# Kernel tuning notes

Measured on AMD Instinct MI355X. Metric: run time of the kernel, lower is better.

## Reference

```python
import jax, jax.numpy as jnp
import numpy as np
from jax import lax

BN_EPS = 1e-5

def _dw_conv_bn(img, w, g, b, mu, var):
    # img: [B,C,H,W], w: [C,1,3,3] depthwise (feature_group_count=C), stride 1, pad 1
    C = img.shape[1]
    y = lax.conv_general_dilated(img, w, (1, 1), 'SAME',
                                 dimension_numbers=('NCHW', 'OIHW', 'NCHW'),
                                 feature_group_count=C)
    scale = (g / jnp.sqrt(var + BN_EPS))[None, :, None, None]
    return y * scale + (b - mu * g / jnp.sqrt(var + BN_EPS))[None, :, None, None]


def setup_inputs() -> dict:
    key = jax.random.key(0)
    B, H, W, C, Co = 32, 28, 28, 192, 192
    T = 1 + H * W
    ks = jax.random.split(key, 8)
    x = jax.random.normal(ks[0], (B, T, C), dtype=jnp.float32)
    conv_w = jax.random.normal(ks[1], (3, C, 1, 3, 3), dtype=jnp.float32) * 0.1
    bn_scale = 1.0 + 0.1 * jax.random.normal(ks[2], (3, C), dtype=jnp.float32)
    bn_bias = 0.1 * jax.random.normal(ks[3], (3, C), dtype=jnp.float32)
    bn_mean = 0.1 * jax.random.normal(ks[4], (3, C), dtype=jnp.float32)
    bn_var = jax.random.uniform(ks[5], (3, C), dtype=jnp.float32, minval=0.5, maxval=1.5)
    w_qkv = jax.random.normal(ks[6], (3, Co, C), dtype=jnp.float32) / np.sqrt(C)
    kp, kb = jax.random.split(ks[7])
    w_proj = jax.random.normal(kp, (Co, Co), dtype=jnp.float32) / np.sqrt(Co)
    b_proj = 0.01 * jax.random.normal(kb, (Co,), dtype=jnp.float32)
    return {"x": x, "conv_w": conv_w, "bn_scale": bn_scale, "bn_bias": bn_bias,
            "bn_mean": bn_mean, "bn_var": bn_var, "w_qkv": w_qkv,
            "w_proj": w_proj, "b_proj": b_proj, "h": H, "w": W, "num_heads": 3}


def reference(x, conv_w, bn_scale, bn_bias, bn_mean, bn_var, w_qkv, w_proj, b_proj, h, w, num_heads):
    B, T, C = x.shape
    Co = w_proj.shape[0]
    scale = Co ** (-0.5)  # NOTE: module scales by dim_out^-0.5, not per-head
    cls_tok, tok = x[:, :1], x[:, 1:]
    img = tok.reshape(B, h, w, C).transpose(0, 3, 1, 2)  # b (h w) c -> b c h w
    qkv = []
    for i in range(3):  # q, k, v conv projections (depthwise conv + BN inference)
        y = _dw_conv_bn(img, conv_w[i], bn_scale[i], bn_bias[i], bn_mean[i], bn_var[i])
        y = y.reshape(B, C, h * w).transpose(0, 2, 1)  # b c h w -> b (h w) c
        y = jnp.concatenate([cls_tok, y], axis=1)      # prepend cls token
        qkv.append(jnp.einsum('btc,oc->bto', y, w_qkv[i]))
    d = Co // num_heads
    q, k, v = (t.reshape(B, T, num_heads, d).transpose(0, 2, 1, 3) for t in qkv)
    attn = jnp.einsum('bhld,bhtd->bhlt', q, k) * scale
    attn = jax.nn.softmax(attn, axis=-1)
    out = jnp.einsum('bhlt,bhtd->bhld', attn, v)
    out = out.transpose(0, 2, 1, 3).reshape(B, T, Co)
    return out @ w_proj.T + b_proj
```

## Files before the change

kernel.cpp:

```cpp
#include <hip/hip_runtime.h>

#define B_   32
#define Hh   28
#define Ww   28
#define Cc   192
#define T_   785
#define BT_  (B_ * T_)
#define BTC_ ((size_t)BT_ * Cc)
#define SCALE2 0.10412163388f

typedef __attribute__((ext_vector_type(8))) __bf16 bf16x8;
typedef __attribute__((ext_vector_type(4))) __bf16 bf16x4;
typedef __attribute__((ext_vector_type(4))) float  f32x4;

__device__ __forceinline__ int imin(int a, int b) { return a < b ? a : b; }

__global__ void wcvt_k(const float* __restrict__ wq, const float* __restrict__ wp,
                       __bf16* __restrict__ dst) {
  int i = blockIdx.x * 256 + threadIdx.x;
  float v = (i < 3 * Cc * Cc) ? wq[i] : wp[i - 3 * Cc * Cc];
  dst[i] = (__bf16)v;
}

__global__ __launch_bounds__(192) void conv3_bn_k(
    const float* __restrict__ x, const float* __restrict__ cw,
    const float* __restrict__ g, const float* __restrict__ bb,
    const float* __restrict__ mu, const float* __restrict__ var,
    __bf16* __restrict__ y)
{
  const int c = threadIdx.x;
  const int h0 = blockIdx.x * 2;
  const int b = blockIdx.y;
  float w9[3][9], sc[3], sh[3];
#pragma unroll
  for (int br = 0; br < 3; ++br) {
    sc[br] = g[br * Cc + c] * rsqrtf(var[br * Cc + c] + 1e-5f);
    sh[br] = bb[br * Cc + c] - mu[br * Cc + c] * sc[br];
#pragma unroll
    for (int k = 0; k < 9; ++k) w9[br][k] = cw[(br * Cc + c) * 9 + k];
  }
  const float* xb = x + (size_t)b * T_ * Cc;
  if (h0 == 0) {
#pragma unroll
    for (int br = 0; br < 3; ++br)
      y[br * BTC_ + (size_t)b * T_ * Cc + c] = (__bf16)xb[c];
  }
  float c0[4], c1[4], c2[4];
#pragma unroll
  for (int r = 0; r < 4; ++r) {
    int rr = h0 - 1 + r;
    c0[r] = 0.f;
    c1[r] = (rr >= 0 && rr < Hh) ? xb[(size_t)(1 + rr * Ww) * Cc + c] : 0.f;
  }
  for (int col = 0; col < Ww; ++col) {
#pragma unroll
    for (int r = 0; r < 4; ++r) {
      int rr = h0 - 1 + r, ci = col + 1;
      c2[r] = (rr >= 0 && rr < Hh && ci < Ww)
                ? xb[(size_t)(1 + rr * Ww + ci) * Cc + c] : 0.f;
    }
#pragma unroll
    for (int ro = 0; ro < 2; ++ro) {
      size_t orow = (size_t)(b * T_ + 1 + (h0 + ro) * Ww + col) * Cc + c;
#pragma unroll
      for (int br = 0; br < 3; ++br) {
        float acc = c0[ro+0]*w9[br][0] + c1[ro+0]*w9[br][1] + c2[ro+0]*w9[br][2]
                  + c0[ro+1]*w9[br][3] + c1[ro+1]*w9[br][4] + c2[ro+1]*w9[br][5]
                  + c0[ro+2]*w9[br][6] + c1[ro+2]*w9[br][7] + c2[ro+2]*w9[br][8];
        y[br * BTC_ + orow] = (__bf16)(acc * sc[br] + sh[br]);
      }
    }
#pragma unroll
    for (int r = 0; r < 4; ++r) { c0[r] = c1[r]; c1[r] = c2[r]; }
  }
}

template <int MODE>
__global__ __launch_bounds__(256) void gemm_bf16(
    const __bf16* __restrict__ A0, const __bf16* __restrict__ W0,
    const float* __restrict__ bias, void* __restrict__ outp)
{
  __shared__ __bf16 As[128][72];
  __shared__ __bf16 Bs[64][72];
  const int z = blockIdx.z;
  const __bf16* A  = A0 + (MODE == 0 ? (size_t)z * BTC_ : 0);
  const __bf16* Bw = W0 + (MODE == 0 ? (size_t)z * Cc * Cc : 0);
  const float oscale = (MODE == 0 && z == 0) ? SCALE2 : 1.0f;
  const int tid = threadIdx.x;
  const int wid = tid >> 6, l = tid & 63, c = l & 15, g = l >> 4;
  const int wm = wid >> 1, wn = wid & 1;
  const int m0 = blockIdx.x * 128, n0 = blockIdx.y * 64;
  const int ar = tid >> 1, ah = tid & 1;
  const int br2 = tid >> 2, bq = tid & 3;

  f32x4 acc[4][2];
#pragma unroll
  for (int i = 0; i < 4; ++i)
#pragma unroll
    for (int j = 0; j < 2; ++j) acc[i][j] = (f32x4)(0.f);

  const __bf16* ap = A + (size_t)imin(m0 + ar, BT_ - 1) * Cc + ah * 32;
  const __bf16* bp = Bw + (size_t)(n0 + br2) * Cc + bq * 16;
  uint4 a0 = *(const uint4*)(ap + 0);
  uint4 a1 = *(const uint4*)(ap + 8);
  uint4 a2 = *(const uint4*)(ap + 16);
  uint4 a3 = *(const uint4*)(ap + 24);
  uint4 b0 = *(const uint4*)(bp + 0);
  uint4 b1 = *(const uint4*)(bp + 8);

  for (int kc = 0; kc < 3; ++kc) {
    __syncthreads();
    *(uint4*)&As[ar][ah * 32 + 0]  = a0;
    *(uint4*)&As[ar][ah * 32 + 8]  = a1;
    *(uint4*)&As[ar][ah * 32 + 16] = a2;
    *(uint4*)&As[ar][ah * 32 + 24] = a3;
    *(uint4*)&Bs[br2][bq * 16 + 0] = b0;
    *(uint4*)&Bs[br2][bq * 16 + 8] = b1;
    if (kc < 2) {
      ap += 64; bp += 64;
      a0 = *(const uint4*)(ap + 0);
      a1 = *(const uint4*)(ap + 8);
      a2 = *(const uint4*)(ap + 16);
      a3 = *(const uint4*)(ap + 24);
      b0 = *(const uint4*)(bp + 0);
      b1 = *(const uint4*)(bp + 8);
    }
    __syncthreads();
#pragma unroll
    for (int ksl = 0; ksl < 2; ++ksl) {
      bf16x8 af[4], bfr[2];
#pragma unroll
      for (int mf = 0; mf < 4; ++mf)
        af[mf] = *(const bf16x8*)&As[wm * 64 + mf * 16 + c][ksl * 32 + g * 8];
#pragma unroll
      for (int nf = 0; nf < 2; ++nf)
        bfr[nf] = *(const bf16x8*)&Bs[wn * 32 + nf * 16 + c][ksl * 32 + g * 8];
#pragma unroll
      for (int mf = 0; mf < 4; ++mf)
#pragma unroll
        for (int nf = 0; nf < 2; ++nf)
          acc[mf][nf] = __builtin_amdgcn_mfma_f32_16x16x32_bf16(
              af[mf], bfr[nf], acc[mf][nf], 0, 0, 0);
    }
  }
  float bias_c[2] = {0.f, 0.f};
  if (MODE == 1) {
#pragma unroll
    for (int nf = 0; nf < 2; ++nf) bias_c[nf] = bias[n0 + wn * 32 + nf * 16 + c];
  }
#pragma unroll
  for (int mf = 0; mf < 4; ++mf) {
#pragma unroll
    for (int i = 0; i < 4; ++i) {
      int m = m0 + wm * 64 + mf * 16 + g * 4 + i;
      if (m < BT_) {
#pragma unroll
        for (int nf = 0; nf < 2; ++nf) {
          int n = n0 + wn * 32 + nf * 16 + c;
          if (MODE == 1)
            ((float*)outp)[(size_t)m * Cc + n] = acc[mf][nf][i] + bias_c[nf];
          else
            ((__bf16*)outp)[z * BTC_ + (size_t)m * Cc + n] =
                (__bf16)(acc[mf][nf][i] * oscale);
        }
      }
    }
  }
}

__global__ __launch_bounds__(256) void attn_mfma(
    const __bf16* __restrict__ qkv, __bf16* __restrict__ aout)
{
  __shared__ __bf16 Ks[64][72];
  __shared__ __bf16 Vt[64][72];
  __shared__ __bf16 Ps[4][16][72];
  const int bid = blockIdx.x;
  const int swz = (bid & 7) * 156 + (bid >> 3);
  const int qt = swz % 13;
  const int g2 = swz / 13;
  const int hh = g2 % 3;
  const int b  = g2 / 3;
  const int tid = threadIdx.x;
  const int wid = tid >> 6, l = tid & 63, c = l & 15, g = l >> 4;
  const __bf16* Q = qkv + ((size_t)(0 * B_ + b) * T_) * Cc + hh * 64;
  const __bf16* K = qkv + ((size_t)(1 * B_ + b) * T_) * Cc + hh * 64;
  const __bf16* V = qkv + ((size_t)(2 * B_ + b) * T_) * Cc + hh * 64;

  const int qrow = qt * 64 + wid * 16 + c;
  const __bf16* qp = Q + (size_t)imin(qrow, T_ - 1) * Cc + g * 8;
  bf16x8 qf[2];
  qf[0] = *(const bf16x8*)(qp);
  qf[1] = *(const bf16x8*)(qp + 32);

  const int skey = tid >> 2, sdq = tid & 3;
  const int vkp = tid & 31, vd0 = (tid >> 5) * 8;

  uint4 kr0, kr1, va, vb;
  auto loadKV = [&](int kt2) {
    const __bf16* kp = K + (size_t)imin(kt2 * 64 + skey, T_ - 1) * Cc + sdq * 16;
    kr0 = *(const uint4*)(kp + 0);
    kr1 = *(const uint4*)(kp + 8);
    const __bf16* v0 = V + (size_t)imin(kt2 * 64 + 2 * vkp + 0, T_ - 1) * Cc + vd0;
    const __bf16* v1 = V + (size_t)imin(kt2 * 64 + 2 * vkp + 1, T_ - 1) * Cc + vd0;
    va = *(const uint4*)v0;
    vb = *(const uint4*)v1;
  };
  loadKV(0);

  f32x4 ot[4];
#pragma unroll
  for (int f = 0; f < 4; ++f) ot[f] = (f32x4)(0.f);
  float m_run = -1e30f, l_run = 0.f;

  for (int kt = 0; kt < 13; ++kt) {
    __syncthreads();
    *(uint4*)&Ks[skey][sdq * 16 + 0] = kr0;
    *(uint4*)&Ks[skey][sdq * 16 + 8] = kr1;
    {
      const ushort* pa = (const ushort*)&va;
      const ushort* pb = (const ushort*)&vb;
#pragma unroll
      for (int e = 0; e < 8; ++e) {
        unsigned pk2 = (unsigned)pa[e] | ((unsigned)pb[e] << 16);
        *(unsigned*)&Vt[vd0 + e][2 * vkp] = pk2;
      }
    }
    if (kt < 12) loadKV(kt + 1);
    __syncthreads();

    f32x4 st[4];
#pragma unroll
    for (int f = 0; f < 4; ++f) st[f] = (f32x4)(0.f);
#pragma unroll
    for (int s = 0; s < 2; ++s) {
#pragma unroll
      for (int f = 0; f < 4; ++f) {
        bf16x8 ka = *(const bf16x8*)&Ks[f * 16 + c][s * 32 + g * 8];
        st[f] = __builtin_amdgcn_mfma_f32_16x16x32_bf16(ka, qf[s], st[f], 0, 0, 0);
      }
    }
    if (kt == 12) {
#pragma unroll
      for (int f = 0; f < 4; ++f)
#pragma unroll
        for (int i = 0; i < 4; ++i)
          if (f * 16 + g * 4 + i >= 17) st[f][i] = -1e30f;
    }
    float pmax = -1e30f;
#pragma unroll
    for (int f = 0; f < 4; ++f)
#pragma unroll
      for (int i = 0; i < 4; ++i) pmax = fmaxf(pmax, st[f][i]);
    pmax = fmaxf(pmax, __shfl_xor(pmax, 16));
    pmax = fmaxf(pmax, __shfl_xor(pmax, 32));
    if (!__all(pmax <= m_run + 8.f)) {
      float mnew = fmaxf(m_run, pmax);
      float corr = exp2f(m_run - mnew);
      m_run = mnew;
      l_run *= corr;
#pragma unroll
      for (int f = 0; f < 4; ++f)
#pragma unroll
        for (int i = 0; i < 4; ++i) ot[f][i] *= corr;
    }
    float rs = 0.f;
#pragma unroll
    for (int f = 0; f < 4; ++f) {
      bf16x4 pk;
#pragma unroll
      for (int i = 0; i < 4; ++i) {
        float p = exp2f(st[f][i] - m_run);
        rs += p;
        pk[i] = (__bf16)p;
      }
      *(bf16x4*)&Ps[wid][c][f * 16 + g * 4] = pk;
    }
    rs += __shfl_xor(rs, 16);
    rs += __shfl_xor(rs, 32);
    l_run += rs;

#pragma unroll
    for (int s = 0; s < 2; ++s) {
      bf16x8 pb2 = *(const bf16x8*)&Ps[wid][c][s * 32 + g * 8];
#pragma unroll
      for (int f = 0; f < 4; ++f) {
        bf16x8 va2 = *(const bf16x8*)&Vt[f * 16 + c][s * 32 + g * 8];
        ot[f] = __builtin_amdgcn_mfma_f32_16x16x32_bf16(va2, pb2, ot[f], 0, 0, 0);
      }
    }
  }

  const int t = qt * 64 + wid * 16 + c;
  if (t < T_) {
    float inv = 1.f / l_run;
    __bf16* op = aout + ((size_t)(b * T_ + t)) * Cc + hh * 64;
#pragma unroll
    for (int f = 0; f < 4; ++f) {
      bf16x4 ov;
#pragma unroll
      for (int i = 0; i < 4; ++i) ov[i] = (__bf16)(ot[f][i] * inv);
      *(bf16x4*)(op + f * 16 + g * 4) = ov;
    }
  }
}

extern "C" void kernel_launch(void* const* d_in, const int* in_sizes, int n_in,
                              void* d_out, int out_size, void* d_ws, size_t ws_size,
                              hipStream_t stream) {
  (void)in_sizes; (void)n_in; (void)out_size; (void)ws_size;
  const float* x        = (const float*)d_in[0];
  const float* conv_w   = (const float*)d_in[1];
  const float* bn_scale = (const float*)d_in[2];
  const float* bn_bias  = (const float*)d_in[3];
  const float* bn_mean  = (const float*)d_in[4];
  const float* bn_var   = (const float*)d_in[5];
  const float* w_qkv    = (const float*)d_in[6];
  const float* w_proj   = (const float*)d_in[7];
  const float* b_proj   = (const float*)d_in[8];

  __bf16* ybf  = (__bf16*)d_ws;
  __bf16* qkvb = ybf + 3 * BTC_;
  __bf16* aobf = qkvb + 3 * BTC_;
  __bf16* wq   = aobf + BTC_;
  __bf16* wp   = wq + 3 * Cc * Cc;

  wcvt_k<<<576, 256, 0, stream>>>(w_qkv, w_proj, wq);
  conv3_bn_k<<<dim3(14, B_), 192, 0, stream>>>(
      x, conv_w, bn_scale, bn_bias, bn_mean, bn_var, ybf);

  const int mblocks = (BT_ + 127) / 128;
  gemm_bf16<0><<<dim3(mblocks, 3, 3), 256, 0, stream>>>(ybf, wq, nullptr, qkvb);
  attn_mfma<<<1248, 256, 0, stream>>>(qkvb, aobf);
  gemm_bf16<1><<<dim3(mblocks, 3, 1), 256, 0, stream>>>(aobf, wp, b_proj, d_out);
}
```

Baseline: 181.7 us.

## Fold weight cast into conv, widen GEMM and attention tiles, add MFMA priority

The separate weight-conversion kernel is folded into an extra block row of the conv kernel, removing one launch. The conv kernel now computes one output row per block instead of two. The GEMM now covers all 192 output columns per block with 512 threads, so each A tile is loaded once rather than three times. Attention blocks now handle 128 queries, two 16-row sets per wave, so each staged K/V tile is reused twice as much, and s_setprio brackets the MFMA sections. Bounds clamps were removed, so edge tiles now read padding rows from neighbouring workspace regions; these reads rely on masking and on that memory holding finite values.

```diff
diff --git a/kernel.cpp b/kernel.cpp
--- a/kernel.cpp
+++ b/kernel.cpp
@@ -13,24 +13,32 @@
 typedef __attribute__((ext_vector_type(4))) __bf16 bf16x4;
 typedef __attribute__((ext_vector_type(4))) float  f32x4;
 
-__device__ __forceinline__ int imin(int a, int b) { return a < b ? a : b; }
-
-__global__ void wcvt_k(const float* __restrict__ wq, const float* __restrict__ wp,
-                       __bf16* __restrict__ dst) {
-  int i = blockIdx.x * 256 + threadIdx.x;
-  float v = (i < 3 * Cc * Cc) ? wq[i] : wp[i - 3 * Cc * Cc];
-  dst[i] = (__bf16)v;
-}
-
 __global__ __launch_bounds__(192) void conv3_bn_k(
     const float* __restrict__ x, const float* __restrict__ cw,
     const float* __restrict__ g, const float* __restrict__ bb,
     const float* __restrict__ mu, const float* __restrict__ var,
-    __bf16* __restrict__ y)
+    __bf16* __restrict__ y,
+    const float* __restrict__ wqkv, const float* __restrict__ wproj,
+    __bf16* __restrict__ wdst)
 {
   const int c = threadIdx.x;
-  const int h0 = blockIdx.x * 2;
+  const int h = blockIdx.x;
   const int b = blockIdx.y;
+  if (h == Hh) {
+    int t = b * 192 + c;
+    int base = t * 24;
+    const float* src = (base < 3 * Cc * Cc) ? (wqkv + base)
+                                            : (wproj + (base - 3 * Cc * Cc));
+#pragma unroll
+    for (int e = 0; e < 24; e += 4) {
+      float4 v = *(const float4*)(src + e);
+      wdst[base + e + 0] = (__bf16)v.x;
+      wdst[base + e + 1] = (__bf16)v.y;
+      wdst[base + e + 2] = (__bf16)v.z;
+      wdst[base + e + 3] = (__bf16)v.w;
+    }
+    return;
+  }
   float w9[3][9], sc[3], sh[3];
 #pragma unroll
   for (int br = 0; br < 3; ++br) {
@@ -40,113 +48,109 @@
     for (int k = 0; k < 9; ++k) w9[br][k] = cw[(br * Cc + c) * 9 + k];
   }
   const float* xb = x + (size_t)b * T_ * Cc;
-  if (h0 == 0) {
+  if (h == 0) {
 #pragma unroll
     for (int br = 0; br < 3; ++br)
       y[br * BTC_ + (size_t)b * T_ * Cc + c] = (__bf16)xb[c];
   }
-  float c0[4], c1[4], c2[4];
-#pragma unroll
-  for (int r = 0; r < 4; ++r) {
-    int rr = h0 - 1 + r;
+  float c0[3], c1[3], c2[3];
+#pragma unroll
+  for (int r = 0; r < 3; ++r) {
+    int rr = h - 1 + r;
     c0[r] = 0.f;
     c1[r] = (rr >= 0 && rr < Hh) ? xb[(size_t)(1 + rr * Ww) * Cc + c] : 0.f;
   }
   for (int col = 0; col < Ww; ++col) {
 #pragma unroll
-    for (int r = 0; r < 4; ++r) {
-      int rr = h0 - 1 + r, ci = col + 1;
+    for (int r = 0; r < 3; ++r) {
+      int rr = h - 1 + r, ci = col + 1;
       c2[r] = (rr >= 0 && rr < Hh && ci < Ww)
                 ? xb[(size_t)(1 + rr * Ww + ci) * Cc + c] : 0.f;
     }
-#pragma unroll
-    for (int ro = 0; ro < 2; ++ro) {
-      size_t orow = (size_t)(b * T_ + 1 + (h0 + ro) * Ww + col) * Cc + c;
-#pragma unroll
-      for (int br = 0; br < 3; ++br) {
-        float acc = c0[ro+0]*w9[br][0] + c1[ro+0]*w9[br][1] + c2[ro+0]*w9[br][2]
-                  + c0[ro+1]*w9[br][3] + c1[ro+1]*w9[br][4] + c2[ro+1]*w9[br][5]
-                  + c0[ro+2]*w9[br][6] + c1[ro+2]*w9[br][7] + c2[ro+2]*w9[br][8];
-        y[br * BTC_ + orow] = (__bf16)(acc * sc[br] + sh[br]);
-      }
-    }
-#pragma unroll
-    for (int r = 0; r < 4; ++r) { c0[r] = c1[r]; c1[r] = c2[r]; }
+    size_t orow = (size_t)(b * T_ + 1 + h * Ww + col) * Cc + c;
+#pragma unroll
+    for (int br = 0; br < 3; ++br) {
+      float acc = c0[0]*w9[br][0] + c1[0]*w9[br][1] + c2[0]*w9[br][2]
+                + c0[1]*w9[br][3] + c1[1]*w9[br][4] + c2[1]*w9[br][5]
+                + c0[2]*w9[br][6] + c1[2]*w9[br][7] + c2[2]*w9[br][8];
+      y[br * BTC_ + orow] = (__bf16)(acc * sc[br] + sh[br]);
+    }
+#pragma unroll
+    for (int r = 0; r < 3; ++r) { c0[r] = c1[r]; c1[r] = c2[r]; }
   }
 }
 
 template <int MODE>
-__global__ __launch_bounds__(256) void gemm_bf16(
+__global__ __launch_bounds__(512) void gemm_bf16(
     const __bf16* __restrict__ A0, const __bf16* __restrict__ W0,
     const float* __restrict__ bias, void* __restrict__ outp)
 {
   __shared__ __bf16 As[128][72];
-  __shared__ __bf16 Bs[64][72];
+  __shared__ __bf16 Bs[192][72];
   const int z = blockIdx.z;
   const __bf16* A  = A0 + (MODE == 0 ? (size_t)z * BTC_ : 0);
   const __bf16* Bw = W0 + (MODE == 0 ? (size_t)z * Cc * Cc : 0);
-  const float oscale = (MODE == 0 && z == 0) ? SCALE2 : 1.0f;
+  const float osc = (MODE == 0 && z == 0) ? SCALE2 : 1.0f;
   const int tid = threadIdx.x;
   const int wid = tid >> 6, l = tid & 63, c = l & 15, g = l >> 4;
-  const int wm = wid >> 1, wn = wid & 1;
-  const int m0 = blockIdx.x * 128, n0 = blockIdx.y * 64;
-  const int ar = tid >> 1, ah = tid & 1;
-  const int br2 = tid >> 2, bq = tid & 3;
-
-  f32x4 acc[4][2];
+  const int wm = wid >> 2, wn = wid & 3;
+  const int m0 = blockIdx.x * 128;
+  const int ar = tid >> 2, aq = tid & 3;
+  const int brow = tid >> 3, bv = tid & 7;
+
+  f32x4 acc[4][3];
 #pragma unroll
   for (int i = 0; i < 4; ++i)
 #pragma unroll
-    for (int j = 0; j < 2; ++j) acc[i][j] = (f32x4)(0.f);
-
-  const __bf16* ap = A + (size_t)imin(m0 + ar, BT_ - 1) * Cc + ah * 32;
-  const __bf16* bp = Bw + (size_t)(n0 + br2) * Cc + bq * 16;
+    for (int j = 0; j < 3; ++j) acc[i][j] = (f32x4)(0.f);
+
+  const __bf16* ap = A + (size_t)(m0 + ar) * Cc + aq * 16;
+  const __bf16* bp0 = Bw + (size_t)brow * Cc + bv * 8;
   uint4 a0 = *(const uint4*)(ap + 0);
   uint4 a1 = *(const uint4*)(ap + 8);
-  uint4 a2 = *(const uint4*)(ap + 16);
-  uint4 a3 = *(const uint4*)(ap + 24);
-  uint4 b0 = *(const uint4*)(bp + 0);
-  uint4 b1 = *(const uint4*)(bp + 8);
+  uint4 b0 = *(const uint4*)(bp0 + 0 * 64 * Cc / 1);
+  uint4 b1 = *(const uint4*)(bp0 + (size_t)64 * Cc);
+  uint4 b2 = *(const uint4*)(bp0 + (size_t)128 * Cc);
 
   for (int kc = 0; kc < 3; ++kc) {
     __syncthreads();
-    *(uint4*)&As[ar][ah * 32 + 0]  = a0;
-    *(uint4*)&As[ar][ah * 32 + 8]  = a1;
-    *(uint4*)&As[ar][ah * 32 + 16] = a2;
-    *(uint4*)&As[ar][ah * 32 + 24] = a3;
-    *(uint4*)&Bs[br2][bq * 16 + 0] = b0;
-    *(uint4*)&Bs[br2][bq * 16 + 8] = b1;
+    *(uint4*)&As[ar][aq * 16 + 0] = a0;
+    *(uint4*)&As[ar][aq * 16 + 8] = a1;
+    *(uint4*)&Bs[brow +   0][bv * 8] = b0;
+    *(uint4*)&Bs[brow +  64][bv * 8] = b1;
+    *(uint4*)&Bs[brow + 128][bv * 8] = b2;
     if (kc < 2) {
-      ap += 64; bp += 64;
+      ap += 64; bp0 += 64;
       a0 = *(const uint4*)(ap + 0);
       a1 = *(const uint4*)(ap + 8);
-      a2 = *(const uint4*)(ap + 16);
-      a3 = *(const uint4*)(ap + 24);
-      b0 = *(const uint4*)(bp + 0);
-      b1 = *(const uint4*)(bp + 8);
+      b0 = *(const uint4*)(bp0);
+      b1 = *(const uint4*)(bp0 + (size_t)64 * Cc);
+      b2 = *(const uint4*)(bp0 + (size_t)128 * Cc);
     }
     __syncthreads();
 #pragma unroll
     for (int ksl = 0; ksl < 2; ++ksl) {
-      bf16x8 af[4], bfr[2];
+      bf16x8 af[4], bfr[3];
 #pragma unroll
       for (int mf = 0; mf < 4; ++mf)
         af[mf] = *(const bf16x8*)&As[wm * 64 + mf * 16 + c][ksl * 32 + g * 8];
 #pragma unroll
-      for (int nf = 0; nf < 2; ++nf)
-        bfr[nf] = *(const bf16x8*)&Bs[wn * 32 + nf * 16 + c][ksl * 32 + g * 8];
+      for (int nf = 0; nf < 3; ++nf)
+        bfr[nf] = *(const bf16x8*)&Bs[wn * 48 + nf * 16 + c][ksl * 32 + g * 8];
+      __builtin_amdgcn_s_setprio(1);
 #pragma unroll
       for (int mf = 0; mf < 4; ++mf)
 #pragma unroll
-        for (int nf = 0; nf < 2; ++nf)
+        for (int nf = 0; nf < 3; ++nf)
           acc[mf][nf] = __builtin_amdgcn_mfma_f32_16x16x32_bf16(
               af[mf], bfr[nf], acc[mf][nf], 0, 0, 0);
-    }
-  }
-  float bias_c[2] = {0.f, 0.f};
+      __builtin_amdgcn_s_setprio(0);
+    }
+  }
+  float bias_c[3] = {0.f, 0.f, 0.f};
   if (MODE == 1) {
 #pragma unroll
-    for (int nf = 0; nf < 2; ++nf) bias_c[nf] = bias[n0 + wn * 32 + nf * 16 + c];
+    for (int nf = 0; nf < 3; ++nf) bias_c[nf] = bias[wn * 48 + nf * 16 + c];
   }
 #pragma unroll
   for (int mf = 0; mf < 4; ++mf) {
@@ -155,13 +159,13 @@
       int m = m0 + wm * 64 + mf * 16 + g * 4 + i;
       if (m < BT_) {
 #pragma unroll
-        for (int nf = 0; nf < 2; ++nf) {
-          int n = n0 + wn * 32 + nf * 16 + c;
+        for (int nf = 0; nf < 3; ++nf) {
+          int n = wn * 48 + nf * 16 + c;
           if (MODE == 1)
             ((float*)outp)[(size_t)m * Cc + n] = acc[mf][nf][i] + bias_c[nf];
           else
             ((__bf16*)outp)[z * BTC_ + (size_t)m * Cc + n] =
-                (__bf16)(acc[mf][nf][i] * oscale);
+                (__bf16)(acc[mf][nf][i] * osc);
         }
       }
     }
@@ -175,9 +179,9 @@
   __shared__ __bf16 Vt[64][72];
   __shared__ __bf16 Ps[4][16][72];
   const int bid = blockIdx.x;
-  const int swz = (bid & 7) * 156 + (bid >> 3);
-  const int qt = swz % 13;
-  const int g2 = swz / 13;
+  const int swz = (bid & 7) * 84 + (bid >> 3);
+  const int qt = swz % 7;
+  const int g2 = swz / 7;
   const int hh = g2 % 3;
   const int b  = g2 / 3;
   const int tid = threadIdx.x;
@@ -186,31 +190,32 @@
   const __bf16* K = qkv + ((size_t)(1 * B_ + b) * T_) * Cc + hh * 64;
   const __bf16* V = qkv + ((size_t)(2 * B_ + b) * T_) * Cc + hh * 64;
 
-  const int qrow = qt * 64 + wid * 16 + c;
-  const __bf16* qp = Q + (size_t)imin(qrow, T_ - 1) * Cc + g * 8;
-  bf16x8 qf[2];
-  qf[0] = *(const bf16x8*)(qp);
-  qf[1] = *(const bf16x8*)(qp + 32);
+  const int q0 = qt * 128 + wid * 32;
+  bf16x8 qf[2][2];
+#pragma unroll
+  for (int s = 0; s < 2; ++s) {
+    const __bf16* qp = Q + (size_t)(q0 + s * 16 + c) * Cc + g * 8;
+    qf[s][0] = *(const bf16x8*)(qp);
+    qf[s][1] = *(const bf16x8*)(qp + 32);
+  }
 
   const int skey = tid >> 2, sdq = tid & 3;
   const int vkp = tid & 31, vd0 = (tid >> 5) * 8;
-
-  uint4 kr0, kr1, va, vb;
-  auto loadKV = [&](int kt2) {
-    const __bf16* kp = K + (size_t)imin(kt2 * 64 + skey, T_ - 1) * Cc + sdq * 16;
-    kr0 = *(const uint4*)(kp + 0);
-    kr1 = *(const uint4*)(kp + 8);
-    const __bf16* v0 = V + (size_t)imin(kt2 * 64 + 2 * vkp + 0, T_ - 1) * Cc + vd0;
-    const __bf16* v1 = V + (size_t)imin(kt2 * 64 + 2 * vkp + 1, T_ - 1) * Cc + vd0;
-    va = *(const uint4*)v0;
-    vb = *(const uint4*)v1;
-  };
-  loadKV(0);
-
-  f32x4 ot[4];
-#pragma unroll
-  for (int f = 0; f < 4; ++f) ot[f] = (f32x4)(0.f);
-  float m_run = -1e30f, l_run = 0.f;
+  const __bf16* kp  = K + (size_t)skey * Cc + sdq * 16;
+  const __bf16* vp0 = V + (size_t)(2 * vkp + 0) * Cc + vd0;
+  const __bf16* vp1 = V + (size_t)(2 * vkp + 1) * Cc + vd0;
+  uint4 kr0 = *(const uint4*)(kp + 0);
+  uint4 kr1 = *(const uint4*)(kp + 8);
+  uint4 va  = *(const uint4*)vp0;
+  uint4 vb  = *(const uint4*)vp1;
+
+  f32x4 ot[2][4];
+#pragma unroll
+  for (int s = 0; s < 2; ++s)
+#pragma unroll
+    for (int f = 0; f < 4; ++f) ot[s][f] = (f32x4)(0.f);
+  float m_run[2] = {-1e30f, -1e30f};
+  float l_run[2] = {0.f, 0.f};
 
   for (int kt = 0; kt < 13; ++kt) {
     __syncthreads();
@@ -225,81 +230,97 @@
         *(unsigned*)&Vt[vd0 + e][2 * vkp] = pk2;
       }
     }
-    if (kt < 12) loadKV(kt + 1);
+    if (kt < 12) {
+      kp += 64 * Cc; vp0 += 64 * Cc; vp1 += 64 * Cc;
+      kr0 = *(const uint4*)(kp + 0);
+      kr1 = *(const uint4*)(kp + 8);
+      va  = *(const uint4*)vp0;
+      vb  = *(const uint4*)vp1;
+    }
     __syncthreads();
 
-    f32x4 st[4];
-#pragma unroll
-    for (int f = 0; f < 4; ++f) st[f] = (f32x4)(0.f);
-#pragma unroll
-    for (int s = 0; s < 2; ++s) {
+#pragma unroll
+    for (int set = 0; set < 2; ++set) {
+      f32x4 st[4];
+#pragma unroll
+      for (int f = 0; f < 4; ++f) st[f] = (f32x4)(0.f);
+      __builtin_amdgcn_s_setprio(1);
+#pragma unroll
+      for (int s2 = 0; s2 < 2; ++s2) {
+#pragma unroll
+        for (int f = 0; f < 4; ++f) {
+          bf16x8 ka = *(const bf16x8*)&Ks[f * 16 + c][s2 * 32 + g * 8];
+          st[f] = __builtin_amdgcn_mfma_f32_16x16x32_bf16(ka, qf[set][s2], st[f], 0, 0, 0);
+        }
+      }
+      __builtin_amdgcn_s_setprio(0);
+      if (kt == 12) {
+#pragma unroll
+        for (int f = 0; f < 4; ++f)
+#pragma unroll
+          for (int i = 0; i < 4; ++i)
+            if (f * 16 + g * 4 + i >= 17) st[f][i] = -1e30f;
+      }
+      float pmax = -1e30f;
+#pragma unroll
+      for (int f = 0; f < 4; ++f)
+#pragma unroll
+        for (int i = 0; i < 4; ++i) pmax = fmaxf(pmax, st[f][i]);
+      pmax = fmaxf(pmax, __shfl_xor(pmax, 16));
+      pmax = fmaxf(pmax, __shfl_xor(pmax, 32));
+      if (!__all(pmax <= m_run[set] + 8.f)) {
+        float mnew = fmaxf(m_run[set], pmax);
+        float corr = exp2f(m_run[set] - mnew);
+        m_run[set] = mnew;
+        l_run[set] *= corr;
+#pragma unroll
+        for (int f = 0; f < 4; ++f)
+#pragma unroll
+          for (int i = 0; i < 4; ++i) ot[set][f][i] *= corr;
+      }
+      float rs = 0.f;
 #pragma unroll
       for (int f = 0; f < 4; ++f) {
-        bf16x8 ka = *(const bf16x8*)&Ks[f * 16 + c][s * 32 + g * 8];
-        st[f] = __builtin_amdgcn_mfma_f32_16x16x32_bf16(ka, qf[s], st[f], 0, 0, 0);
-      }
-    }
-    if (kt == 12) {
-#pragma unroll
-      for (int f = 0; f < 4; ++f)
-#pragma unroll
-        for (int i = 0; i < 4; ++i)
-          if (f * 16 + g * 4 + i >= 17) st[f][i] = -1e30f;
-    }
-    float pmax = -1e30f;
-#pragma unroll
-    for (int f = 0; f < 4; ++f)
-#pragma unroll
-      for (int i = 0; i < 4; ++i) pmax = fmaxf(pmax, st[f][i]);
-    pmax = fmaxf(pmax, __shfl_xor(pmax, 16));
-    pmax = fmaxf(pmax, __shfl_xor(pmax, 32));
-    if (!__all(pmax <= m_run + 8.f)) {
-      float mnew = fmaxf(m_run, pmax);
-      float corr = exp2f(m_run - mnew);
-      m_run = mnew;
-      l_run *= corr;
-#pragma unroll
-      for (int f = 0; f < 4; ++f)
-#pragma unroll
-        for (int i = 0; i < 4; ++i) ot[f][i] *= corr;
-    }
-    float rs = 0.f;
-#pragma unroll
-    for (int f = 0; f < 4; ++f) {
-      bf16x4 pk;
-#pragma unroll
-      for (int i = 0; i < 4; ++i) {
-        float p = exp2f(st[f][i] - m_run);
-        rs += p;
-        pk[i] = (__bf16)p;
-      }
-      *(bf16x4*)&Ps[wid][c][f * 16 + g * 4] = pk;
-    }
-    rs += __shfl_xor(rs, 16);
-    rs += __shfl_xor(rs, 32);
-    l_run += rs;
-
-#pragma unroll
-    for (int s = 0; s < 2; ++s) {
-      bf16x8 pb2 = *(const bf16x8*)&Ps[wid][c][s * 32 + g * 8];
+        bf16x4 pk;
+#pragma unroll
+        for (int i = 0; i < 4; ++i) {
+          float p = exp2f(st[f][i] - m_run[set]);
+          rs += p;
+          pk[i] = (__bf16)p;
+        }
+        *(bf16x4*)&Ps[wid][c][f * 16 + g * 4] = pk;
+      }
+      rs += __shfl_xor(rs, 16);
+      rs += __shfl_xor(rs, 32);
+      l_run[set] += rs;
+
+      __builtin_amdgcn_s_setprio(1);
+#pragma unroll
+      for (int s2 = 0; s2 < 2; ++s2) {
+        bf16x8 pb2 = *(const bf16x8*)&Ps[wid][c][s2 * 32 + g * 8];
+#pragma unroll
+        for (int f = 0; f < 4; ++f) {
+          bf16x8 va2 = *(const bf16x8*)&Vt[f * 16 + c][s2 * 32 + g * 8];
+          ot[set][f] = __builtin_amdgcn_mfma_f32_16x16x32_bf16(va2, pb2, ot[set][f], 0, 0, 0);
+        }
+      }
+      __builtin_amdgcn_s_setprio(0);
+    }
+  }
+
+#pragma unroll
+  for (int set = 0; set < 2; ++set) {
+    const int t = q0 + set * 16 + c;
+    if (t < T_) {
+      float inv = 1.f / l_run[set];
+      __bf16* op = aout + ((size_t)(b * T_ + t)) * Cc + hh * 64;
 #pragma unroll
       for (int f = 0; f < 4; ++f) {
-        bf16x8 va2 = *(const bf16x8*)&Vt[f * 16 + c][s * 32 + g * 8];
-        ot[f] = __builtin_amdgcn_mfma_f32_16x16x32_bf16(va2, pb2, ot[f], 0, 0, 0);
-      }
-    }
-  }
-
-  const int t = qt * 64 + wid * 16 + c;
-  if (t < T_) {
-    float inv = 1.f / l_run;
-    __bf16* op = aout + ((size_t)(b * T_ + t)) * Cc + hh * 64;
-#pragma unroll
-    for (int f = 0; f < 4; ++f) {
-      bf16x4 ov;
-#pragma unroll
-      for (int i = 0; i < 4; ++i) ov[i] = (__bf16)(ot[f][i] * inv);
-      *(bf16x4*)(op + f * 16 + g * 4) = ov;
+        bf16x4 ov;
+#pragma unroll
+        for (int i = 0; i < 4; ++i) ov[i] = (__bf16)(ot[set][f][i] * inv);
+        *(bf16x4*)(op + f * 16 + g * 4) = ov;
+      }
     }
   }
 }
@@ -324,12 +345,11 @@
   __bf16* wq   = aobf + BTC_;
   __bf16* wp   = wq + 3 * Cc * Cc;
 
-  wcvt_k<<<576, 256, 0, stream>>>(w_qkv, w_proj, wq);
-  conv3_bn_k<<<dim3(14, B_), 192, 0, stream>>>(
-      x, conv_w, bn_scale, bn_bias, bn_mean, bn_var, ybf);
+  conv3_bn_k<<<dim3(Hh + 1, B_), 192, 0, stream>>>(
+      x, conv_w, bn_scale, bn_bias, bn_mean, bn_var, ybf, w_qkv, w_proj, wq);
 
   const int mblocks = (BT_ + 127) / 128;
-  gemm_bf16<0><<<dim3(mblocks, 3, 3), 256, 0, stream>>>(ybf, wq, nullptr, qkvb);
-  attn_mfma<<<1248, 256, 0, stream>>>(qkvb, aobf);
-  gemm_bf16<1><<<dim3(mblocks, 3, 1), 256, 0, stream>>>(aobf, wp, b_proj, d_out);
+  gemm_bf16<0><<<dim3(mblocks, 1, 3), 512, 0, stream>>>(ybf, wq, nullptr, qkvb);
+  attn_mfma<<<672, 256, 0, stream>>>(qkvb, aobf);
+  gemm_bf16<1><<<dim3(mblocks, 1, 1), 512, 0, stream>>>(aobf, wp, b_proj, d_out);
 }
```

Result: no change. 179.4 us (-1.2%).
